# Performance work log

Hardware: AMD Instinct MI355X
Metric: run time of the kernel (lower is better)

Reference implementation:

```python
import jax, jax.numpy as jnp
import numpy as np


def setup_inputs() -> dict:
    key = jax.random.key(0)
    ks = jax.random.split(key, 8)
    B, T, M, A, H, O = 64, 256, 16, 32, 64, 1
    return {
        "x_m": jax.random.uniform(ks[0], (B, T, M), dtype=jnp.float32),
        "x_a": jax.random.normal(ks[1], (B, T, A), dtype=jnp.float32),
        "Wj": jax.random.normal(ks[2], (M * H, A), dtype=jnp.float32) * 0.1,
        "bj": jnp.zeros((M * H,), jnp.float32),
        "Wr": jax.random.normal(ks[3], (H * H, A), dtype=jnp.float32) * 0.1,
        "br": jnp.zeros((H * H,), jnp.float32),
        "Wo": jax.random.normal(ks[4], (H, A), dtype=jnp.float32) * 0.1,
        "bo": jnp.full((H,), -3.0, jnp.float32),  # out_gate bias init -3
        "Wfc": jax.random.normal(ks[5], (O, H), dtype=jnp.float32) * 0.1,
        "bfc": jnp.zeros((O,), jnp.float32),
    }


def reference(x_m, x_a, Wj, bj, Wr, br, Wo, bo, Wfc, bfc):
    B, T, Mm = x_m.shape
    H = Wo.shape[0]
    # Precompute input-dependent gates for all timesteps (they only depend on x_a)
    J = jax.nn.softmax((x_a @ Wj.T + bj).reshape(B, T, Mm, H), axis=-1)   # junction
    R = jax.nn.softmax((x_a @ Wr.T + br).reshape(B, T, H, H), axis=-1)    # redistribution
    Og = jax.nn.sigmoid(x_a @ Wo.T + bo)                                   # out gate [B,T,H]
    m_in = jnp.einsum('btm,btmh->bth', x_m, J)                             # mass inflow

    # time-first for scan
    m_in_t = jnp.moveaxis(m_in, 1, 0)   # [T,B,H]
    R_t = jnp.moveaxis(R, 1, 0)         # [T,B,H,H]
    O_t = jnp.moveaxis(Og, 1, 0)        # [T,B,H]

    def step(c, inp):
        mi, r, o = inp
        m_new = mi + jnp.einsum('bh,bhk->bk', c, r)
        c_new = (1.0 - o) * m_new
        return c_new, (o * m_new, c_new)

    c0 = jnp.zeros((B, H), x_m.dtype)
    _, (m_out, c_seq) = jax.lax.scan(step, c0, (m_in_t, R_t, O_t))

    pred = m_out[-1] @ Wfc.T + bfc          # fc on last timestep output
    c = jnp.moveaxis(c_seq, 0, 1)           # [B,T,H]
    return pred, c
```

## Files before the change

kernel.cpp:

```cpp
#include <hip/hip_runtime.h>

constexpr int B = 64, T = 256, M = 16, A = 32, H = 64;
constexpr int ROWB = 11264;
constexpr int S = 32;
constexpr int NBLK = T / S;

typedef __attribute__((ext_vector_type(8))) short bf16x8;
typedef __attribute__((ext_vector_type(4))) float f32x4;
typedef _Float16 half2 __attribute__((ext_vector_type(2)));
typedef __fp16 fp16x2 __attribute__((ext_vector_type(2)));
typedef _Float16 f16x8 __attribute__((ext_vector_type(8)));

constexpr size_t OW  = 0;
constexpr size_t OX  = 332800;
constexpr size_t OB  = 1381376;
constexpr size_t OXM = 1402880;
constexpr size_t OG  = 1927168;
constexpr size_t OP  = OG + (size_t)B * T * ROWB;
constexpr size_t OC  = OP + (size_t)B * NBLK * 64 * 144;

template<int N> __device__ __forceinline__ void vmwait() {
    asm volatile("s_waitcnt vmcnt(%0)" :: "n"(N) : "memory");
}
__device__ __forceinline__ float dot2(unsigned a, unsigned b, float c) {
    return __builtin_amdgcn_fdot2(__builtin_bit_cast(half2, a),
                                  __builtin_bit_cast(half2, b), c, false);
}
__device__ __forceinline__ unsigned pkrtz(float a, float b) {
    fp16x2 pk = __builtin_amdgcn_cvt_pkrtz(a, b);
    return __builtin_bit_cast(unsigned, pk);
}
__device__ __forceinline__ float h2f(unsigned u) {
    return (float)__builtin_bit_cast(_Float16, (unsigned short)(u & 0xffffu));
}

__global__ __launch_bounds__(256) void prep_kernel(
    const float* __restrict__ x_a, const float* __restrict__ x_m,
    const float* __restrict__ Wj, const float* __restrict__ Wr,
    const float* __restrict__ Wo,
    const float* __restrict__ bj, const float* __restrict__ br,
    const float* __restrict__ bo, unsigned char* ws)
{
    const int nW = 5184 * 32, nX = B * T * A, nXM = B * T * M, nB = 5184;
    int idx = blockIdx.x * 256 + threadIdx.x;
    if (idx >= nW + nX + nXM + nB) return;
    if (idx < nW + nX) {
        float v; ushort* dst;
        if (idx < nW) {
            int row = idx >> 5;
            v = (row < 1024) ? Wj[idx] : (row < 5120) ? Wr[idx - 1024 * 32] : Wo[idx - 5120 * 32];
            dst = (ushort*)(ws + OW) + idx;
        } else {
            v = x_a[idx - nW];
            dst = (ushort*)(ws + OX) + (idx - nW);
        }
        unsigned u = __builtin_bit_cast(unsigned, v);
        *dst = (ushort)((u + 0x7fffu + ((u >> 16) & 1u)) >> 16);
    } else if (idx < nW + nX + nXM) {
        int j = idx - nW - nX;
        ((_Float16*)(ws + OXM))[j] = (_Float16)x_m[j];
    } else {
        int row = idx - nW - nX - nXM;
        float v = (row < 1024) ? bj[row] : (row < 5120) ? br[row - 1024] : bo[row - 5120];
        ((float*)(ws + OB))[row] = v;
    }
}

__global__ __launch_bounds__(128) void gate_kernel(unsigned char* ws)
{
    const int tid = threadIdx.x, l = tid & 63, wv = tid >> 6;
    const int l15 = l & 15, l4 = l >> 4;
    const ushort* Wb = (const ushort*)(ws + OW);
    const ushort* xb = (const ushort*)(ws + OX);
    const float*  bc = (const float*)(ws + OB);
    unsigned char* G = ws + OG;

    __shared__ __align__(16) unsigned char tile[2 * 16 * 1040];
    unsigned char* wtile = tile + wv * 16 * 1040;

    const int r0 = blockIdx.x * 16;
    const bf16x8 bx = *(const bf16x8*)(xb + (size_t)(r0 + l15) * 32 + l4 * 8);
    const f32x4 zero = {0.f, 0.f, 0.f, 0.f};

    const int no = (wv == 0) ? 6 : 5;
    for (int oi = 0; oi < no; ++oi) {
        const int oct = oi * 2 + wv;

        if (oct < 10) {
            f32x4 s[4];
            #pragma unroll
            for (int gi = 0; gi < 8; ++gi) {
                const int g = oct * 8 + gi;
                f32x4 d[4];
                #pragma unroll
                for (int ct = 0; ct < 4; ++ct) {
                    const bf16x8 aW = *(const bf16x8*)(
                        Wb + (size_t)(g * 64 + ct * 16 + l15) * 32 + l4 * 8);
                    d[ct] = __builtin_amdgcn_mfma_f32_16x16x32_bf16(aW, bx, zero, 0, 0, 0);
                    const float4 bv = *(const float4*)(bc + g * 64 + ct * 16 + l4 * 4);
                    d[ct][0] += bv.x; d[ct][1] += bv.y; d[ct][2] += bv.z; d[ct][3] += bv.w;
                }
                {
                    float sm = 0.f;
                    #pragma unroll
                    for (int ct = 0; ct < 4; ++ct)
                        #pragma unroll
                        for (int j = 0; j < 4; ++j) { d[ct][j] = __expf(d[ct][j]); sm += d[ct][j]; }
                    sm += __shfl_xor(sm, 16); sm += __shfl_xor(sm, 32);
                    const float inv = __fdividef(1.f, sm);
                    #pragma unroll
                    for (int ct = 0; ct < 4; ++ct)
                        #pragma unroll
                        for (int j = 0; j < 4; ++j) d[ct][j] *= inv;
                }
                if (gi & 1) {
                    const int p = gi >> 1;
                    #pragma unroll
                    for (int ct = 0; ct < 4; ++ct)
                        #pragma unroll
                        for (int j = 0; j < 4; ++j) {
                            const int gc = ct * 16 + l4 * 4 + j;
                            *(unsigned*)(wtile + l15 * 1040 + gc * 16 + p * 4) =
                                pkrtz(s[ct][j], d[ct][j]);
                        }
                } else {
                    #pragma unroll
                    for (int ct = 0; ct < 4; ++ct) s[ct] = d[ct];
                }
            }
        } else {
            f32x4 d[4];
            #pragma unroll
            for (int ct = 0; ct < 4; ++ct) {
                const bf16x8 aW = *(const bf16x8*)(
                    Wb + (size_t)(80 * 64 + ct * 16 + l15) * 32 + l4 * 8);
                d[ct] = __builtin_amdgcn_mfma_f32_16x16x32_bf16(aW, bx, zero, 0, 0, 0);
                const float4 bv = *(const float4*)(bc + 80 * 64 + ct * 16 + l4 * 4);
                d[ct][0] += bv.x; d[ct][1] += bv.y; d[ct][2] += bv.z; d[ct][3] += bv.w;
                #pragma unroll
                for (int j = 0; j < 4; ++j)
                    d[ct][j] = __fdividef(1.f, 1.f + __expf(-d[ct][j]));
            }
            #pragma unroll
            for (int ct = 0; ct < 4; ++ct)
                #pragma unroll
                for (int j = 0; j < 4; ++j) {
                    const int gc = ct * 16 + l4 * 4 + j;
                    unsigned u = pkrtz(d[ct][j], d[ct][j]);
                    unsigned char* base = wtile + l15 * 1040 + gc * 16;
                    *(unsigned*)(base + 0)  = u; *(unsigned*)(base + 4)  = u;
                    *(unsigned*)(base + 8)  = u; *(unsigned*)(base + 12) = u;
                }
        }

        asm volatile("s_waitcnt lgkmcnt(0)" ::: "memory");
        __builtin_amdgcn_sched_barrier(0);
        #pragma unroll
        for (int t = 0; t < 16; ++t) {
            uint4 v = *(const uint4*)(wtile + t * 1040 + l * 16);
            *(uint4*)(G + (size_t)(r0 + t) * ROWB + oct * 1024 + l * 16) = v;
        }
        asm volatile("s_waitcnt lgkmcnt(0)" ::: "memory");
        __builtin_amdgcn_sched_barrier(0);
    }
}

__global__ __launch_bounds__(256, 2) void compose_kernel(unsigned char* ws)
{
    const int tid = threadIdx.x, l = tid & 63, wv = tid >> 6;
    const int l15 = l & 15, l4 = l >> 4;
    const unsigned char* G = ws + OG;

    __shared__ __align__(16) unsigned char P_lds[8 * 1296];
    __shared__ __align__(16) float d_lds[64];
    __shared__ __align__(16) float dD_lds[64];
    __shared__ __align__(16) unsigned xs[256];

    const int bb = blockIdx.x >> 3, blk = blockIdx.x & 7;
    const size_t row0 = (size_t)bb * T + blk * S;
    const uint4* xq = (const uint4*)xs;

    if (tid < 64)
        ((uint4*)xs)[tid] = ((const uint4*)(ws + OXM + row0 * 32))[tid];

    float acc[5][4];
    #pragma unroll
    for (int ct = 0; ct < 5; ++ct)
        #pragma unroll
        for (int j = 0; j < 4; ++j) {
            const int r = wv * 16 + l4 * 4 + j, c = ct * 16 + l15;
            acc[ct][j] = (r == c) ? 1.f : 0.f;
        }
    __syncthreads();

    uint4 A0n, A1n, J0n, J1n; unsigned on_ = 0;
    {
        const unsigned char* rp = G + row0 * ROWB;
        A0n = *(const uint4*)(rp + 2048 + l4 * 1024 + (wv * 16 + l15) * 16);
        A1n = *(const uint4*)(rp + 2048 + (4 + l4) * 1024 + (wv * 16 + l15) * 16);
        if (wv == 0) {
            J0n = *(const uint4*)(rp + l * 16);
            J1n = *(const uint4*)(rp + 1024 + l * 16);
            on_ = *(const ushort*)(rp + 10240 + l * 16);
        }
    }

    for (int tc = 0; tc < S; ++tc) {
        const uint4 A0 = A0n, A1 = A1n, J0 = J0n, J1 = J1n;
        const unsigned ou = on_;

        #pragma unroll
        for (int ct = 0; ct < 5; ++ct) {
            const int hoct = wv * 2 + (l4 >> 1);
            *(uint2*)(P_lds + hoct * 1296 + (ct * 16 + l15) * 16 + (l4 & 1) * 8) =
                make_uint2(pkrtz(acc[ct][0], acc[ct][1]), pkrtz(acc[ct][2], acc[ct][3]));
        }
        if (wv == 0) {
            const uint4 X0 = xq[tc * 2], X1 = xq[tc * 2 + 1];
            float m = 0.f;
            m = dot2(X0.x, J0.x, m); m = dot2(X0.y, J0.y, m);
            m = dot2(X0.z, J0.z, m); m = dot2(X0.w, J0.w, m);
            m = dot2(X1.x, J1.x, m); m = dot2(X1.y, J1.y, m);
            m = dot2(X1.z, J1.z, m); m = dot2(X1.w, J1.w, m);
            const float dD = 1.f - h2f(ou);
            d_lds[l] = dD * m;
            dD_lds[l] = dD;
        }
        asm volatile("s_waitcnt lgkmcnt(0)" ::: "memory");
        __builtin_amdgcn_s_barrier();

        if (tc + 1 < S) {
            const unsigned char* rp = G + (row0 + tc + 1) * ROWB;
            A0n = *(const uint4*)(rp + 2048 + l4 * 1024 + (wv * 16 + l15) * 16);
            A1n = *(const uint4*)(rp + 2048 + (4 + l4) * 1024 + (wv * 16 + l15) * 16);
            if (wv == 0) {
                J0n = *(const uint4*)(rp + l * 16);
                J1n = *(const uint4*)(rp + 1024 + l * 16);
                on_ = *(const ushort*)(rp + 10240 + l * 16);
            }
        }

        const f16x8 a0 = __builtin_bit_cast(f16x8, A0);
        const f16x8 a1 = __builtin_bit_cast(f16x8, A1);
        f32x4 dn[5];
        #pragma unroll
        for (int ct = 0; ct < 5; ++ct) {
            const f16x8 b0 = *(const f16x8*)(P_lds + l4 * 1296 + (ct * 16 + l15) * 16);
            const f16x8 b1 = *(const f16x8*)(P_lds + (4 + l4) * 1296 + (ct * 16 + l15) * 16);
            f32x4 z = {0.f, 0.f, 0.f, 0.f};
            z = __builtin_amdgcn_mfma_f32_16x16x32_f16(a0, b0, z, 0, 0, 0);
            z = __builtin_amdgcn_mfma_f32_16x16x32_f16(a1, b1, z, 0, 0, 0);
            dn[ct] = z;
        }
        const int rb = wv * 16 + l4 * 4;
        const float dd0 = dD_lds[rb], dd1 = dD_lds[rb + 1];
        const float dd2 = dD_lds[rb + 2], dd3 = dD_lds[rb + 3];
        #pragma unroll
        for (int ct = 0; ct < 5; ++ct) {
            acc[ct][0] = dn[ct][0] * dd0; acc[ct][1] = dn[ct][1] * dd1;
            acc[ct][2] = dn[ct][2] * dd2; acc[ct][3] = dn[ct][3] * dd3;
        }
        if (l15 == 0) {
            acc[4][0] += d_lds[rb];     acc[4][1] += d_lds[rb + 1];
            acc[4][2] += d_lds[rb + 2]; acc[4][3] += d_lds[rb + 3];
        }
        asm volatile("s_waitcnt lgkmcnt(0)" ::: "memory");
        __builtin_amdgcn_s_barrier();
    }

    unsigned char* pb = ws + OP + (size_t)blockIdx.x * 9216;
    #pragma unroll
    for (int ct = 0; ct < 5; ++ct) {
        if (ct == 4 && l15 != 0) continue;
        #pragma unroll
        for (int j = 0; j < 4; ++j) {
            const int r = wv * 16 + l4 * 4 + j, c = ct * 16 + l15;
            *(_Float16*)(pb + r * 144 + c * 2) = (_Float16)acc[ct][j];
        }
    }
}

__global__ __launch_bounds__(64, 1) void prop_kernel(unsigned char* ws)
{
    const int b = blockIdx.x, l = threadIdx.x;
    __shared__ __align__(16) unsigned cpk[32];

    _Float16* OCp = (_Float16*)(ws + OC);
    float cn = 0.f;
    if (l < 32) cpk[l] = 0;
    asm volatile("s_waitcnt lgkmcnt(0)" ::: "memory");

    for (int blk = 0; blk < NBLK; ++blk) {
        OCp[(size_t)(b * NBLK + blk) * 64 + l] = (_Float16)cn;
        if (blk == NBLK - 1) break;

        const unsigned char* prow = ws + OP + (size_t)(b * NBLK + blk) * 9216 + l * 144;
        uint4 p[8];
        #pragma unroll
        for (int i = 0; i < 8; ++i) p[i] = *(const uint4*)(prow + i * 16);
        const float q = h2f(*(const ushort*)(prow + 128));

        const uint4 C0 = ((const uint4*)cpk)[0], C1 = ((const uint4*)cpk)[1];
        const uint4 C2 = ((const uint4*)cpk)[2], C3 = ((const uint4*)cpk)[3];
        const uint4 C4 = ((const uint4*)cpk)[4], C5 = ((const uint4*)cpk)[5];
        const uint4 C6 = ((const uint4*)cpk)[6], C7 = ((const uint4*)cpk)[7];

        float a0 = q, a1 = 0.f, a2 = 0.f, a3 = 0.f;
        a0 = dot2(C0.x, p[0].x, a0); a0 = dot2(C0.y, p[0].y, a0);
        a0 = dot2(C0.z, p[0].z, a0); a0 = dot2(C0.w, p[0].w, a0);
        a1 = dot2(C1.x, p[1].x, a1); a1 = dot2(C1.y, p[1].y, a1);
        a1 = dot2(C1.z, p[1].z, a1); a1 = dot2(C1.w, p[1].w, a1);
        a2 = dot2(C2.x, p[2].x, a2); a2 = dot2(C2.y, p[2].y, a2);
        a2 = dot2(C2.z, p[2].z, a2); a2 = dot2(C2.w, p[2].w, a2);
        a3 = dot2(C3.x, p[3].x, a3); a3 = dot2(C3.y, p[3].y, a3);
        a3 = dot2(C3.z, p[3].z, a3); a3 = dot2(C3.w, p[3].w, a3);
        a0 = dot2(C4.x, p[4].x, a0); a0 = dot2(C4.y, p[4].y, a0);
        a0 = dot2(C4.z, p[4].z, a0); a0 = dot2(C4.w, p[4].w, a0);
        a1 = dot2(C5.x, p[5].x, a1); a1 = dot2(C5.y, p[5].y, a1);
        a1 = dot2(C5.z, p[5].z, a1); a1 = dot2(C5.w, p[5].w, a1);
        a2 = dot2(C6.x, p[6].x, a2); a2 = dot2(C6.y, p[6].y, a2);
        a2 = dot2(C6.z, p[6].z, a2); a2 = dot2(C6.w, p[6].w, a2);
        a3 = dot2(C7.x, p[7].x, a3); a3 = dot2(C7.y, p[7].y, a3);
        a3 = dot2(C7.z, p[7].z, a3); a3 = dot2(C7.w, p[7].w, a3);
        cn = (a0 + a1) + (a2 + a3);

        asm volatile("s_waitcnt lgkmcnt(0)" ::: "memory");
        __builtin_amdgcn_sched_barrier(0);
        ((_Float16*)cpk)[l] = (_Float16)cn;
        asm volatile("s_waitcnt lgkmcnt(0)" ::: "memory");
        __builtin_amdgcn_sched_barrier(0);
    }
}

__global__ __launch_bounds__(64, 1) void scan_kernel(
    const unsigned char* __restrict__ ws,
    const float* __restrict__ Wfc, const float* __restrict__ bfc,
    float* __restrict__ out)
{
    const int b = blockIdx.x >> 3, blk = blockIdx.x & 7;
    const int l = threadIdx.x;
    const int t00 = blk * S;
    const unsigned char* G = ws + OG;

    __shared__ __align__(16) unsigned char buf[6][ROWB];
    __shared__ __align__(16) unsigned xs[256];
    __shared__ __align__(16) unsigned c_pk[32];

    float* cbase = out + B;

    if (l < 64)
        ((uint4*)xs)[l] = ((const uint4*)(ws + OXM + ((size_t)b * T + t00) * 32))[l];
    if (l < 32)
        c_pk[l] = *(const unsigned*)(ws + OC + (size_t)blockIdx.x * 128 + l * 4);
    const float wfck = Wfc[l];
    const float bfc0 = bfc[0];
    asm volatile("s_waitcnt vmcnt(0) lgkmcnt(0)" ::: "memory");

#define DMA(tc_, bi_)                                                           \
    {                                                                           \
        const unsigned char* rp_ = G + ((size_t)b * T + t00 + (tc_)) * ROWB;    \
        unsigned char* lb_ = &buf[bi_][0];                                      \
        _Pragma("unroll")                                                       \
        for (int i_ = 0; i_ < 11; ++i_)                                         \
            __builtin_amdgcn_global_load_lds(                                   \
                (const __attribute__((address_space(1))) unsigned int*)         \
                    (rp_ + i_ * 1024 + l * 16),                                 \
                (__attribute__((address_space(3))) unsigned int*)               \
                    (lb_ + i_ * 1024), 16, 0, 0);                               \
    }

    DMA(0, 0); DMA(1, 1); DMA(2, 2); DMA(3, 3); DMA(4, 4); DMA(5, 5);

    const uint4* cq = (const uint4*)c_pk;
    const uint4* xq = (const uint4*)xs;
    int bi = 0;

    for (int tc = 0; tc < S; ++tc) {
        const int rem = (S - 1) - tc;
        if (tc >= 5) {
            if      (rem >= 5) vmwait<60>();
            else if (rem == 4) vmwait<49>();
            else if (rem == 3) vmwait<38>();
            else if (rem == 2) vmwait<27>();
            else if (rem == 1) vmwait<16>();
            else               vmwait<5>();
        } else {
            if      (tc == 0) vmwait<55>();
            else if (tc == 1) vmwait<56>();
            else if (tc == 2) vmwait<57>();
            else if (tc == 3) vmwait<58>();
            else              vmwait<59>();
        }
        __builtin_amdgcn_sched_barrier(0);

        const unsigned char* bp = &buf[bi][0];

        const uint4 J0 = *(const uint4*)(bp + l * 16);
        const uint4 J1 = *(const uint4*)(bp + 1024 + l * 16);
        const uint4 R0 = *(const uint4*)(bp + 2048 + l * 16);
        const uint4 R1 = *(const uint4*)(bp + 3072 + l * 16);
        const uint4 R2 = *(const uint4*)(bp + 4096 + l * 16);
        const uint4 R3 = *(const uint4*)(bp + 5120 + l * 16);
        const uint4 R4 = *(const uint4*)(bp + 6144 + l * 16);
        const uint4 R5 = *(const uint4*)(bp + 7168 + l * 16);
        const uint4 R6 = *(const uint4*)(bp + 8192 + l * 16);
        const uint4 R7 = *(const uint4*)(bp + 9216 + l * 16);
        const float o = h2f(*(const ushort*)(bp + 10240 + l * 16));

        const uint4 X0 = xq[tc * 2], X1 = xq[tc * 2 + 1];
        const uint4 C0 = cq[0], C1 = cq[1], C2 = cq[2], C3 = cq[3];
        const uint4 C4 = cq[4], C5 = cq[5], C6 = cq[6], C7 = cq[7];

        float a0 = 0.f, a1 = 0.f, a2 = 0.f, a3 = 0.f;
        a0 = dot2(X0.x, J0.x, a0); a0 = dot2(X0.y, J0.y, a0);
        a0 = dot2(X0.z, J0.z, a0); a0 = dot2(X0.w, J0.w, a0);
        a1 = dot2(X1.x, J1.x, a1); a1 = dot2(X1.y, J1.y, a1);
        a1 = dot2(X1.z, J1.z, a1); a1 = dot2(X1.w, J1.w, a1);
        a0 = dot2(C0.x, R0.x, a0); a0 = dot2(C0.y, R0.y, a0);
        a0 = dot2(C0.z, R0.z, a0); a0 = dot2(C0.w, R0.w, a0);
        a0 = dot2(C1.x, R1.x, a0); a0 = dot2(C1.y, R1.y, a0);
        a0 = dot2(C1.z, R1.z, a0); a0 = dot2(C1.w, R1.w, a0);
        a1 = dot2(C2.x, R2.x, a1); a1 = dot2(C2.y, R2.y, a1);
        a1 = dot2(C2.z, R2.z, a1); a1 = dot2(C2.w, R2.w, a1);
        a1 = dot2(C3.x, R3.x, a1); a1 = dot2(C3.y, R3.y, a1);
        a1 = dot2(C3.z, R3.z, a1); a1 = dot2(C3.w, R3.w, a1);
        a2 = dot2(C4.x, R4.x, a2); a2 = dot2(C4.y, R4.y, a2);
        a2 = dot2(C4.z, R4.z, a2); a2 = dot2(C4.w, R4.w, a2);
        a2 = dot2(C5.x, R5.x, a2); a2 = dot2(C5.y, R5.y, a2);
        a2 = dot2(C5.z, R5.z, a2); a2 = dot2(C5.w, R5.w, a2);
        a3 = dot2(C6.x, R6.x, a3); a3 = dot2(C6.y, R6.y, a3);
        a3 = dot2(C6.z, R6.z, a3); a3 = dot2(C6.w, R6.w, a3);
        a3 = dot2(C7.x, R7.x, a3); a3 = dot2(C7.y, R7.y, a3);
        a3 = dot2(C7.z, R7.z, a3); a3 = dot2(C7.w, R7.w, a3);

        const float m_new = (a0 + a1) + (a2 + a3);
        const float cn = (1.f - o) * m_new;

        cbase[((size_t)b * T + t00 + tc) * H + l] = cn;
        ((_Float16*)c_pk)[l] = (_Float16)cn;

        if (blk == NBLK - 1 && tc == S - 1) {
            float v = o * m_new * wfck;
            v += __shfl_xor(v, 1);  v += __shfl_xor(v, 2);
            v += __shfl_xor(v, 4);  v += __shfl_xor(v, 8);
            v += __shfl_xor(v, 16); v += __shfl_xor(v, 32);
            if (l == 0) out[b] = v + bfc0;
        }

        asm volatile("s_waitcnt lgkmcnt(0)" ::: "memory");
        __builtin_amdgcn_sched_barrier(0);

        if (tc + 6 < S) DMA(tc + 6, bi);
        bi = (bi == 5) ? 0 : bi + 1;
    }
#undef DMA
}

extern "C" void kernel_launch(void* const* d_in, const int* in_sizes, int n_in,
                              void* d_out, int out_size, void* d_ws, size_t ws_size,
                              hipStream_t stream) {
    const float* x_m = (const float*)d_in[0];
    const float* x_a = (const float*)d_in[1];
    const float* Wj  = (const float*)d_in[2];
    const float* bj  = (const float*)d_in[3];
    const float* Wr  = (const float*)d_in[4];
    const float* br  = (const float*)d_in[5];
    const float* Wo  = (const float*)d_in[6];
    const float* bo  = (const float*)d_in[7];
    const float* Wfc = (const float*)d_in[8];
    const float* bfc = (const float*)d_in[9];
    float* out = (float*)d_out;
    unsigned char* ws = (unsigned char*)d_ws;

    {
        const int total = 5184 * 32 + B * T * A + B * T * M + 5184;
        prep_kernel<<<(total + 255) / 256, 256, 0, stream>>>(
            x_a, x_m, Wj, Wr, Wo, bj, br, bo, ws);
    }
    gate_kernel<<<(B * T) / 16, 128, 0, stream>>>(ws);
    compose_kernel<<<B * NBLK, 256, 0, stream>>>(ws);
    prop_kernel<<<B, 64, 0, stream>>>(ws);
    scan_kernel<<<B * NBLK, 64, 0, stream>>>(ws, Wfc, bfc, out);
}
```

Baseline: 117.2 us.

## Fold junction softmax and mass inflow into gate kernel, shrink gate rows

The gate kernel now reduces the junction softmax against x_m itself, producing m_in per (row, h) and packing it with the out-gate as an fp16 pair. The full J tensor and the replicated out-gate bytes are no longer written to the workspace. The per-row gate record shrinks from 11264 to 8448 bytes, which cuts global write and read traffic and LDS DMA work in the compose and scan kernels and removes their x_m staging and J dot products. In exchange the gate kernel gains extra LDS reductions and two block syncs, and m_in is rounded to fp16 after accumulation.

```diff
diff --git a/kernel.cpp b/kernel.cpp
--- a/kernel.cpp
+++ b/kernel.cpp
@@ -1,7 +1,7 @@
 #include <hip/hip_runtime.h>
 
 constexpr int B = 64, T = 256, M = 16, A = 32, H = 64;
-constexpr int ROWB = 11264;
+constexpr int ROWB = 8448;
 constexpr int S = 32;
 constexpr int NBLK = T / S;
 
@@ -18,6 +18,7 @@
 constexpr size_t OG  = 1927168;
 constexpr size_t OP  = OG + (size_t)B * T * ROWB;
 constexpr size_t OC  = OP + (size_t)B * NBLK * 64 * 144;
+
 
 template<int N> __device__ __forceinline__ void vmwait() {
     asm volatile("s_waitcnt vmcnt(%0)" :: "n"(N) : "memory");
@@ -76,81 +77,138 @@
     unsigned char* G = ws + OG;
 
     __shared__ __align__(16) unsigned char tile[2 * 16 * 1040];
+    __shared__ __align__(16) float pml[1024];
+    __shared__ _Float16 ol[1024];
+    __shared__ _Float16 xm_lds[256];
     unsigned char* wtile = tile + wv * 16 * 1040;
 
     const int r0 = blockIdx.x * 16;
     const bf16x8 bx = *(const bf16x8*)(xb + (size_t)(r0 + l15) * 32 + l4 * 8);
     const f32x4 zero = {0.f, 0.f, 0.f, 0.f};
 
-    const int no = (wv == 0) ? 6 : 5;
-    for (int oi = 0; oi < no; ++oi) {
-        const int oct = oi * 2 + wv;
-
-        if (oct < 10) {
-            f32x4 s[4];
+    {
+        ((unsigned*)xm_lds)[tid] = ((const unsigned*)(ws + OXM + (size_t)r0 * 32))[tid];
+    }
+    __syncthreads();
+
+    float xmr[8];
+    #pragma unroll
+    for (int ji = 0; ji < 8; ++ji)
+        xmr[ji] = (float)xm_lds[l15 * 16 + wv * 8 + ji];
+
+    float pm[4][4];
+    #pragma unroll
+    for (int ct = 0; ct < 4; ++ct)
+        #pragma unroll
+        for (int j = 0; j < 4; ++j) pm[ct][j] = 0.f;
+
+    #pragma unroll
+    for (int ji = 0; ji < 8; ++ji) {
+        const int g = wv * 8 + ji;
+        f32x4 d[4];
+        #pragma unroll
+        for (int ct = 0; ct < 4; ++ct) {
+            const bf16x8 aW = *(const bf16x8*)(
+                Wb + (size_t)(g * 64 + ct * 16 + l15) * 32 + l4 * 8);
+            d[ct] = __builtin_amdgcn_mfma_f32_16x16x32_bf16(aW, bx, zero, 0, 0, 0);
+            const float4 bv = *(const float4*)(bc + g * 64 + ct * 16 + l4 * 4);
+            d[ct][0] += bv.x; d[ct][1] += bv.y; d[ct][2] += bv.z; d[ct][3] += bv.w;
+        }
+        float sm = 0.f;
+        #pragma unroll
+        for (int ct = 0; ct < 4; ++ct)
             #pragma unroll
-            for (int gi = 0; gi < 8; ++gi) {
-                const int g = oct * 8 + gi;
-                f32x4 d[4];
-                #pragma unroll
-                for (int ct = 0; ct < 4; ++ct) {
-                    const bf16x8 aW = *(const bf16x8*)(
-                        Wb + (size_t)(g * 64 + ct * 16 + l15) * 32 + l4 * 8);
-                    d[ct] = __builtin_amdgcn_mfma_f32_16x16x32_bf16(aW, bx, zero, 0, 0, 0);
-                    const float4 bv = *(const float4*)(bc + g * 64 + ct * 16 + l4 * 4);
-                    d[ct][0] += bv.x; d[ct][1] += bv.y; d[ct][2] += bv.z; d[ct][3] += bv.w;
-                }
-                {
-                    float sm = 0.f;
-                    #pragma unroll
-                    for (int ct = 0; ct < 4; ++ct)
-                        #pragma unroll
-                        for (int j = 0; j < 4; ++j) { d[ct][j] = __expf(d[ct][j]); sm += d[ct][j]; }
-                    sm += __shfl_xor(sm, 16); sm += __shfl_xor(sm, 32);
-                    const float inv = __fdividef(1.f, sm);
-                    #pragma unroll
-                    for (int ct = 0; ct < 4; ++ct)
-                        #pragma unroll
-                        for (int j = 0; j < 4; ++j) d[ct][j] *= inv;
-                }
-                if (gi & 1) {
-                    const int p = gi >> 1;
-                    #pragma unroll
-                    for (int ct = 0; ct < 4; ++ct)
-                        #pragma unroll
-                        for (int j = 0; j < 4; ++j) {
-                            const int gc = ct * 16 + l4 * 4 + j;
-                            *(unsigned*)(wtile + l15 * 1040 + gc * 16 + p * 4) =
-                                pkrtz(s[ct][j], d[ct][j]);
-                        }
-                } else {
-                    #pragma unroll
-                    for (int ct = 0; ct < 4; ++ct) s[ct] = d[ct];
-                }
+            for (int j = 0; j < 4; ++j) { d[ct][j] = __expf(d[ct][j]); sm += d[ct][j]; }
+        sm += __shfl_xor(sm, 16); sm += __shfl_xor(sm, 32);
+        const float inv = __fdividef(xmr[ji], sm);
+        #pragma unroll
+        for (int ct = 0; ct < 4; ++ct)
+            #pragma unroll
+            for (int j = 0; j < 4; ++j) pm[ct][j] += inv * d[ct][j];
+    }
+
+    if (wv == 1) {
+        f32x4 d[4];
+        #pragma unroll
+        for (int ct = 0; ct < 4; ++ct) {
+            const bf16x8 aW = *(const bf16x8*)(
+                Wb + (size_t)(80 * 64 + ct * 16 + l15) * 32 + l4 * 8);
+            d[ct] = __builtin_amdgcn_mfma_f32_16x16x32_bf16(aW, bx, zero, 0, 0, 0);
+            const float4 bv = *(const float4*)(bc + 80 * 64 + ct * 16 + l4 * 4);
+            d[ct][0] += bv.x; d[ct][1] += bv.y; d[ct][2] += bv.z; d[ct][3] += bv.w;
+            #pragma unroll
+            for (int j = 0; j < 4; ++j) {
+                const int gc = ct * 16 + l4 * 4 + j;
+                ol[l15 * 64 + gc] =
+                    (_Float16)__fdividef(1.f, 1.f + __expf(-d[ct][j]));
             }
-        } else {
+        }
+    } else {
+        #pragma unroll
+        for (int ct = 0; ct < 4; ++ct)
+            *(float4*)&pml[l15 * 64 + ct * 16 + l4 * 4] =
+                make_float4(pm[ct][0], pm[ct][1], pm[ct][2], pm[ct][3]);
+    }
+    __syncthreads();
+    if (wv == 1) {
+        #pragma unroll
+        for (int ct = 0; ct < 4; ++ct) {
+            float4 v = *(const float4*)&pml[l15 * 64 + ct * 16 + l4 * 4];
+            *(float4*)&pml[l15 * 64 + ct * 16 + l4 * 4] = make_float4(
+                v.x + pm[ct][0], v.y + pm[ct][1], v.z + pm[ct][2], v.w + pm[ct][3]);
+        }
+    }
+    __syncthreads();
+
+    #pragma unroll
+    for (int i = 0; i < 8; ++i) {
+        const int idx = i * 128 + tid;
+        const int t = idx >> 6, k = idx & 63;
+        *(unsigned*)(G + (size_t)(r0 + t) * ROWB + 8192 + k * 4) =
+            pkrtz(pml[idx], (float)ol[idx]);
+    }
+
+    for (int i = 0; i < 4; ++i) {
+        const int ro = 2 * i + wv;
+        f32x4 s[4];
+        #pragma unroll
+        for (int gi = 0; gi < 8; ++gi) {
+            const int g = 16 + ro * 8 + gi;
             f32x4 d[4];
             #pragma unroll
             for (int ct = 0; ct < 4; ++ct) {
                 const bf16x8 aW = *(const bf16x8*)(
-                    Wb + (size_t)(80 * 64 + ct * 16 + l15) * 32 + l4 * 8);
+                    Wb + (size_t)(g * 64 + ct * 16 + l15) * 32 + l4 * 8);
                 d[ct] = __builtin_amdgcn_mfma_f32_16x16x32_bf16(aW, bx, zero, 0, 0, 0);
-                const float4 bv = *(const float4*)(bc + 80 * 64 + ct * 16 + l4 * 4);
+                const float4 bv = *(const float4*)(bc + g * 64 + ct * 16 + l4 * 4);
                 d[ct][0] += bv.x; d[ct][1] += bv.y; d[ct][2] += bv.z; d[ct][3] += bv.w;
-                #pragma unroll
-                for (int j = 0; j < 4; ++j)
-                    d[ct][j] = __fdividef(1.f, 1.f + __expf(-d[ct][j]));
             }
+            float sm = 0.f;
             #pragma unroll
             for (int ct = 0; ct < 4; ++ct)
                 #pragma unroll
-                for (int j = 0; j < 4; ++j) {
-                    const int gc = ct * 16 + l4 * 4 + j;
-                    unsigned u = pkrtz(d[ct][j], d[ct][j]);
-                    unsigned char* base = wtile + l15 * 1040 + gc * 16;
-                    *(unsigned*)(base + 0)  = u; *(unsigned*)(base + 4)  = u;
-                    *(unsigned*)(base + 8)  = u; *(unsigned*)(base + 12) = u;
-                }
+                for (int j = 0; j < 4; ++j) { d[ct][j] = __expf(d[ct][j]); sm += d[ct][j]; }
+            sm += __shfl_xor(sm, 16); sm += __shfl_xor(sm, 32);
+            const float inv = __fdividef(1.f, sm);
+            #pragma unroll
+            for (int ct = 0; ct < 4; ++ct)
+                #pragma unroll
+                for (int j = 0; j < 4; ++j) d[ct][j] *= inv;
+
+            if (gi & 1) {
+                const int p = gi >> 1;
+                #pragma unroll
+                for (int ct = 0; ct < 4; ++ct)
+                    #pragma unroll
+                    for (int j = 0; j < 4; ++j) {
+                        const int gc = ct * 16 + l4 * 4 + j;
+                        *(unsigned*)(wtile + l15 * 1040 + gc * 16 + p * 4) =
+                            pkrtz(s[ct][j], d[ct][j]);
+                    }
+            } else {
+                #pragma unroll
+                for (int ct = 0; ct < 4; ++ct) s[ct] = d[ct];
+            }
         }
 
         asm volatile("s_waitcnt lgkmcnt(0)" ::: "memory");
@@ -158,7 +216,7 @@
         #pragma unroll
         for (int t = 0; t < 16; ++t) {
             uint4 v = *(const uint4*)(wtile + t * 1040 + l * 16);
-            *(uint4*)(G + (size_t)(r0 + t) * ROWB + oct * 1024 + l * 16) = v;
+            *(uint4*)(G + (size_t)(r0 + t) * ROWB + ro * 1024 + l * 16) = v;
         }
         asm volatile("s_waitcnt lgkmcnt(0)" ::: "memory");
         __builtin_amdgcn_sched_barrier(0);
@@ -174,14 +232,9 @@
     __shared__ __align__(16) unsigned char P_lds[8 * 1296];
     __shared__ __align__(16) float d_lds[64];
     __shared__ __align__(16) float dD_lds[64];
-    __shared__ __align__(16) unsigned xs[256];
 
     const int bb = blockIdx.x >> 3, blk = blockIdx.x & 7;
     const size_t row0 = (size_t)bb * T + blk * S;
-    const uint4* xq = (const uint4*)xs;
-
-    if (tid < 64)
-        ((uint4*)xs)[tid] = ((const uint4*)(ws + OXM + row0 * 32))[tid];
 
     float acc[5][4];
     #pragma unroll
@@ -191,23 +244,18 @@
             const int r = wv * 16 + l4 * 4 + j, c = ct * 16 + l15;
             acc[ct][j] = (r == c) ? 1.f : 0.f;
         }
-    __syncthreads();
-
-    uint4 A0n, A1n, J0n, J1n; unsigned on_ = 0;
+
+    uint4 A0n, A1n; unsigned mon = 0;
     {
         const unsigned char* rp = G + row0 * ROWB;
-        A0n = *(const uint4*)(rp + 2048 + l4 * 1024 + (wv * 16 + l15) * 16);
-        A1n = *(const uint4*)(rp + 2048 + (4 + l4) * 1024 + (wv * 16 + l15) * 16);
-        if (wv == 0) {
-            J0n = *(const uint4*)(rp + l * 16);
-            J1n = *(const uint4*)(rp + 1024 + l * 16);
-            on_ = *(const ushort*)(rp + 10240 + l * 16);
-        }
+        A0n = *(const uint4*)(rp + l4 * 1024 + (wv * 16 + l15) * 16);
+        A1n = *(const uint4*)(rp + (4 + l4) * 1024 + (wv * 16 + l15) * 16);
+        if (wv == 0) mon = *(const unsigned*)(rp + 8192 + l * 4);
     }
 
     for (int tc = 0; tc < S; ++tc) {
-        const uint4 A0 = A0n, A1 = A1n, J0 = J0n, J1 = J1n;
-        const unsigned ou = on_;
+        const uint4 A0 = A0n, A1 = A1n;
+        const unsigned mo = mon;
 
         #pragma unroll
         for (int ct = 0; ct < 5; ++ct) {
@@ -216,14 +264,8 @@
                 make_uint2(pkrtz(acc[ct][0], acc[ct][1]), pkrtz(acc[ct][2], acc[ct][3]));
         }
         if (wv == 0) {
-            const uint4 X0 = xq[tc * 2], X1 = xq[tc * 2 + 1];
-            float m = 0.f;
-            m = dot2(X0.x, J0.x, m); m = dot2(X0.y, J0.y, m);
-            m = dot2(X0.z, J0.z, m); m = dot2(X0.w, J0.w, m);
-            m = dot2(X1.x, J1.x, m); m = dot2(X1.y, J1.y, m);
-            m = dot2(X1.z, J1.z, m); m = dot2(X1.w, J1.w, m);
-            const float dD = 1.f - h2f(ou);
-            d_lds[l] = dD * m;
+            const float dD = 1.f - h2f(mo >> 16);
+            d_lds[l] = dD * h2f(mo);
             dD_lds[l] = dD;
         }
         asm volatile("s_waitcnt lgkmcnt(0)" ::: "memory");
@@ -231,13 +273,9 @@
 
         if (tc + 1 < S) {
             const unsigned char* rp = G + (row0 + tc + 1) * ROWB;
-            A0n = *(const uint4*)(rp + 2048 + l4 * 1024 + (wv * 16 + l15) * 16);
-            A1n = *(const uint4*)(rp + 2048 + (4 + l4) * 1024 + (wv * 16 + l15) * 16);
-            if (wv == 0) {
-                J0n = *(const uint4*)(rp + l * 16);
-                J1n = *(const uint4*)(rp + 1024 + l * 16);
-                on_ = *(const ushort*)(rp + 10240 + l * 16);
-            }
+            A0n = *(const uint4*)(rp + l4 * 1024 + (wv * 16 + l15) * 16);
+            A1n = *(const uint4*)(rp + (4 + l4) * 1024 + (wv * 16 + l15) * 16);
+            if (wv == 0) mon = *(const unsigned*)(rp + 8192 + l * 4);
         }
 
         const f16x8 a0 = __builtin_bit_cast(f16x8, A0);
@@ -343,13 +381,10 @@
     const unsigned char* G = ws + OG;
 
     __shared__ __align__(16) unsigned char buf[6][ROWB];
-    __shared__ __align__(16) unsigned xs[256];
     __shared__ __align__(16) unsigned c_pk[32];
 
     float* cbase = out + B;
 
-    if (l < 64)
-        ((uint4*)xs)[l] = ((const uint4*)(ws + OXM + ((size_t)b * T + t00) * 32))[l];
     if (l < 32)
         c_pk[l] = *(const unsigned*)(ws + OC + (size_t)blockIdx.x * 128 + l * 4);
     const float wfck = Wfc[l];
@@ -361,61 +396,60 @@
         const unsigned char* rp_ = G + ((size_t)b * T + t00 + (tc_)) * ROWB;    \
         unsigned char* lb_ = &buf[bi_][0];                                      \
         _Pragma("unroll")                                                       \
-        for (int i_ = 0; i_ < 11; ++i_)                                         \
+        for (int i_ = 0; i_ < 8; ++i_)                                          \
             __builtin_amdgcn_global_load_lds(                                   \
                 (const __attribute__((address_space(1))) unsigned int*)         \
                     (rp_ + i_ * 1024 + l * 16),                                 \
                 (__attribute__((address_space(3))) unsigned int*)               \
                     (lb_ + i_ * 1024), 16, 0, 0);                               \
+        __builtin_amdgcn_global_load_lds(                                       \
+            (const __attribute__((address_space(1))) unsigned int*)             \
+                (rp_ + 8192 + l * 4),                                           \
+            (__attribute__((address_space(3))) unsigned int*)                   \
+                (lb_ + 8192), 4, 0, 0);                                         \
     }
 
     DMA(0, 0); DMA(1, 1); DMA(2, 2); DMA(3, 3); DMA(4, 4); DMA(5, 5);
 
     const uint4* cq = (const uint4*)c_pk;
-    const uint4* xq = (const uint4*)xs;
     int bi = 0;
 
     for (int tc = 0; tc < S; ++tc) {
-        const int rem = (S - 1) - tc;
-        if (tc >= 5) {
-            if      (rem >= 5) vmwait<60>();
-            else if (rem == 4) vmwait<49>();
-            else if (rem == 3) vmwait<38>();
-            else if (rem == 2) vmwait<27>();
-            else if (rem == 1) vmwait<16>();
+        if (tc >= 6) {
+            const int rem = (S - 1) - tc;
+            if      (rem >= 5) vmwait<50>();
+            else if (rem == 4) vmwait<41>();
+            else if (rem == 3) vmwait<32>();
+            else if (rem == 2) vmwait<23>();
+            else if (rem == 1) vmwait<14>();
             else               vmwait<5>();
         } else {
-            if      (tc == 0) vmwait<55>();
-            else if (tc == 1) vmwait<56>();
-            else if (tc == 2) vmwait<57>();
-            else if (tc == 3) vmwait<58>();
-            else              vmwait<59>();
+            if      (tc == 0) vmwait<45>();
+            else if (tc == 1) vmwait<46>();
+            else if (tc == 2) vmwait<47>();
+            else if (tc == 3) vmwait<48>();
+            else if (tc == 4) vmwait<49>();
+            else              vmwait<50>();
         }
         __builtin_amdgcn_sched_barrier(0);
 
         const unsigned char* bp = &buf[bi][0];
 
-        const uint4 J0 = *(const uint4*)(bp + l * 16);
-        const uint4 J1 = *(const uint4*)(bp + 1024 + l * 16);
-        const uint4 R0 = *(const uint4*)(bp + 2048 + l * 16);
-        const uint4 R1 = *(const uint4*)(bp + 3072 + l * 16);
-        const uint4 R2 = *(const uint4*)(bp + 4096 + l * 16);
-        const uint4 R3 = *(const uint4*)(bp + 5120 + l * 16);
-        const uint4 R4 = *(const uint4*)(bp + 6144 + l * 16);
-        const uint4 R5 = *(const uint4*)(bp + 7168 + l * 16);
-        const uint4 R6 = *(const uint4*)(bp + 8192 + l * 16);
-        const uint4 R7 = *(const uint4*)(bp + 9216 + l * 16);
-        const float o = h2f(*(const ushort*)(bp + 10240 + l * 16));
-
-        const uint4 X0 = xq[tc * 2], X1 = xq[tc * 2 + 1];
+        const uint4 R0 = *(const uint4*)(bp + 0    + l * 16);
+        const uint4 R1 = *(const uint4*)(bp + 1024 + l * 16);
+        const uint4 R2 = *(const uint4*)(bp + 2048 + l * 16);
+        const uint4 R3 = *(const uint4*)(bp + 3072 + l * 16);
+        const uint4 R4 = *(const uint4*)(bp + 4096 + l * 16);
+        const uint4 R5 = *(const uint4*)(bp + 5120 + l * 16);
+        const uint4 R6 = *(const uint4*)(bp + 6144 + l * 16);
+        const uint4 R7 = *(const uint4*)(bp + 7168 + l * 16);
+        const unsigned mo = *(const unsigned*)(bp + 8192 + l * 4);
+        const float o = h2f(mo >> 16);
+
         const uint4 C0 = cq[0], C1 = cq[1], C2 = cq[2], C3 = cq[3];
         const uint4 C4 = cq[4], C5 = cq[5], C6 = cq[6], C7 = cq[7];
 
-        float a0 = 0.f, a1 = 0.f, a2 = 0.f, a3 = 0.f;
-        a0 = dot2(X0.x, J0.x, a0); a0 = dot2(X0.y, J0.y, a0);
-        a0 = dot2(X0.z, J0.z, a0); a0 = dot2(X0.w, J0.w, a0);
-        a1 = dot2(X1.x, J1.x, a1); a1 = dot2(X1.y, J1.y, a1);
-        a1 = dot2(X1.z, J1.z, a1); a1 = dot2(X1.w, J1.w, a1);
+        float a0 = h2f(mo), a1 = 0.f, a2 = 0.f, a3 = 0.f;
         a0 = dot2(C0.x, R0.x, a0); a0 = dot2(C0.y, R0.y, a0);
         a0 = dot2(C0.z, R0.z, a0); a0 = dot2(C0.w, R0.w, a0);
         a0 = dot2(C1.x, R1.x, a0); a0 = dot2(C1.y, R1.y, a0);
```

New measurement: 107.0 us. -8.7%, faster.
